# Kernel optimization log

Measured on AMD Instinct MI355X. Metric: run time of the kernel, lower is better.

The kernel has to match this reference:

```python
import jax, jax.numpy as jnp
import numpy as np

N = 100000   # nodes
E = 1600000  # edges
H = 150      # hidden_dim
G = 256      # num graphs in batch
L = 5        # num_layers
GATE_H = 200


def setup_inputs() -> dict:
    key = jax.random.key(0)
    ks = jax.random.split(key, 12)
    s = lambda k, shape, fan: jax.random.normal(k, shape, dtype=jnp.float32) / np.sqrt(fan)
    return {
        "x": jax.random.normal(ks[0], (N, H), dtype=jnp.float32),
        "edge_index": jax.random.randint(ks[1], (2, E), 0, N, dtype=jnp.int64),
        "batch": jnp.sort(jax.random.randint(ks[2], (N,), 0, G, dtype=jnp.int64)),
        "W": s(ks[3], (L, H, H), H),              # GatedGraphConv per-layer weight
        "w_ih": s(ks[4], (3 * H, H), H),           # GRUCell input weights (r,z,n)
        "w_hh": s(ks[5], (3 * H, H), H),
        "b_ih": jnp.zeros((3 * H,), jnp.float32),
        "b_hh": jnp.zeros((3 * H,), jnp.float32),
        "gw1": s(ks[6], (H, GATE_H), H),           # gate_nn Linear(150,200)
        "gb1": jnp.zeros((GATE_H,), jnp.float32),
        "gw2": s(ks[7], (GATE_H, 1), GATE_H),      # gate_nn Linear(200,1)
        "gb2": jnp.zeros((1,), jnp.float32),
    }


def _gru_cell(m, h, w_ih, w_hh, b_ih, b_hh):
    gi = m @ w_ih.T + b_ih   # [N, 3H]
    gh = h @ w_hh.T + b_hh
    ir, iz, inn = jnp.split(gi, 3, axis=-1)
    hr, hz, hn = jnp.split(gh, 3, axis=-1)
    r = jax.nn.sigmoid(ir + hr)
    z = jax.nn.sigmoid(iz + hz)
    n = jnp.tanh(inn + r * hn)
    return (1.0 - z) * n + z * h


def reference(x, edge_index, batch, W, w_ih, w_hh, b_ih, b_hh, gw1, gb1, gw2, gb2):
    src, dst = edge_index[0], edge_index[1]
    h = x
    # GatedGraphConv: per layer, linear transform, scatter_add aggregation, GRU update
    for i in range(L):
        m = h @ W[i]                                   # [N, H]
        agg = jax.ops.segment_sum(m[src], dst, num_segments=N)  # scatter_add over edges
        h = _gru_cell(agg, h, w_ih, w_hh, b_ih, b_hh)
    # GlobalAttention readout
    gate = jnp.tanh(h @ gw1 + gb1) @ gw2 + gb2          # [N, 1]
    gmax = jax.ops.segment_max(gate, batch, num_segments=G)    # [G, 1]
    gate = jnp.exp(gate - gmax[batch])
    gsum = jax.ops.segment_sum(gate, batch, num_segments=G)    # [G, 1]
    gate = gate / (gsum[batch] + 1e-16)                 # segment softmax
    out = jax.ops.segment_sum(gate * h, batch, num_segments=G)  # [G, H]
    return out, gate
```

## Files before the change

### kernel.cpp

```cpp
#include <hip/hip_runtime.h>
#include <math.h>

#define NN 100000
#define NE 1600000
#define H 150
#define NG 256
#define NL 5
#define GH 200
#define HS 160
#define LS 168
#define CHN 1563
#define CH2 782
#define SNB 98
#define CSRMAX 2304000

typedef unsigned short u16;
typedef unsigned int   u32;
typedef __attribute__((ext_vector_type(8))) short bf16x8;
typedef __attribute__((ext_vector_type(4))) float f32x4;

__device__ __forceinline__ float bf2f(u32 lo16){ u32 t = lo16 << 16; return __builtin_bit_cast(float, t); }
__device__ __forceinline__ u16 f2bf(float f){
  u32 u = __builtin_bit_cast(u32, f);
  u += 0x7fffu + ((u >> 16) & 1u);
  return (u16)(u >> 16);
}
__device__ __forceinline__ u32 pack2(float a, float b){ return (u32)f2bf(a) | ((u32)f2bf(b) << 16); }
__device__ __forceinline__ float fast_sig(float x){
  float e = __expf(-x);
  return __builtin_amdgcn_rcpf(1.f + e);
}
__device__ __forceinline__ float fast_tanh(float x){
  float cx = fminf(fmaxf(x, -15.f), 15.f);
  float e = __expf(2.f*cx);
  return (e - 1.f) * __builtin_amdgcn_rcpf(e + 1.f);
}

__global__ void k_hist(const int* __restrict__ ed, int* __restrict__ cnt){
  int e = blockIdx.x*256 + threadIdx.x;
  if (e < NE) atomicAdd(&cnt[ed[e]], 1);
}

__global__ __launch_bounds__(256) void k_scan1(const int* __restrict__ cnt, int* __restrict__ part){
  __shared__ int red[256];
  const int b = blockIdx.x, tid = threadIdx.x;
  const int base = b*1024;
  int s = 0;
  #pragma unroll
  for (int i = 0; i < 4; ++i){
    int idx = base + tid + i*256;
    int v = (idx < NN) ? cnt[idx] : 0;
    s += (v + 7) & ~7;
  }
  red[tid] = s; __syncthreads();
  for (int st = 128; st >= 1; st >>= 1){
    if (tid < st) red[tid] += red[tid+st];
    __syncthreads();
  }
  if (tid == 0) part[b] = red[0];
}

__global__ void k_scan2(int* __restrict__ part){
  const int t = threadIdx.x;
  int v0 = (2*t   < SNB) ? part[2*t]   : 0;
  int v1 = (2*t+1 < SNB) ? part[2*t+1] : 0;
  int s = v0 + v1, x = s;
  #pragma unroll
  for (int off = 1; off < 64; off <<= 1){
    int tt = __shfl_up(x, off);
    if (t >= off) x += tt;
  }
  int excl = x - s;
  if (2*t   < SNB) part[2*t]   = excl;
  if (2*t+1 < SNB) part[2*t+1] = excl + v0;
}

__global__ __launch_bounds__(1024) void k_scan3(const int* __restrict__ cnt,
        const int* __restrict__ part, int* __restrict__ rowptr, int* __restrict__ cursor){
  __shared__ int wsum[16];
  const int b = blockIdx.x, tid = threadIdx.x;
  const int wid = tid >> 6, lane = tid & 63;
  const int idx = b*1024 + tid;
  int c = (idx < NN) ? cnt[idx] : 0;
  int v = (c + 7) & ~7;
  int x = v;
  #pragma unroll
  for (int off = 1; off < 64; off <<= 1){
    int t = __shfl_up(x, off);
    if (lane >= off) x += t;
  }
  if (lane == 63) wsum[wid] = x;
  __syncthreads();
  if (tid < 16){
    int s = wsum[tid];
    int y = s;
    #pragma unroll
    for (int off = 1; off < 16; off <<= 1){
      int t = __shfl_up(y, off);
      if (tid >= off) y += t;
    }
    wsum[tid] = y - s;
  }
  __syncthreads();
  if (idx < NN){
    int incl = part[b] + wsum[wid] + x;
    rowptr[idx+1] = incl;
    cursor[idx]   = incl - v;
  }
  if (idx == 0) rowptr[0] = 0;
}

__global__ __launch_bounds__(256) void k_pre(int* __restrict__ csr){
  int i = (blockIdx.x*256 + threadIdx.x)*4;
  int4 v = {NN, NN, NN, NN};
  *(int4*)&csr[i] = v;
}

__global__ void k_fill(const int* __restrict__ es, const int* __restrict__ ed,
                       int* __restrict__ cursor, int* __restrict__ csr){
  int e = blockIdx.x*256 + threadIdx.x;
  if (e < NE){
    int pos = atomicAdd(&cursor[ed[e]], 1);
    csr[pos] = es[e];
  }
}

__global__ __launch_bounds__(256) void k_wc(const float* __restrict__ W,
        const float* __restrict__ wih, float* __restrict__ Wc){
  int idx = blockIdx.x*256 + threadIdx.x;
  if (idx >= NL*H*450) return;
  int l = idx / (H*450);
  int rem = idx - l*H*450;
  int k = rem / 450;
  int j = rem - k*450;
  const float* Wr = W   + (size_t)l*H*H + (size_t)k*H;
  const float* wr = wih + (size_t)j*H;
  float acc = 0.f;
  for (int t = 0; t < H; ++t) acc = fmaf(Wr[t], wr[t], acc);
  Wc[idx] = acc;
}

__global__ void k_packi(const float* __restrict__ Wc, short* __restrict__ wbi){
  int idx = blockIdx.x*256 + threadIdx.x;
  int li = idx & 511;
  int q = idx >> 9;
  int mat = q % 3; q /= 3;
  int ks = q % 5;  q /= 5;
  int ct = q % 10; int l = q / 10;
  int lane = li >> 3, j = li & 7;
  int k = ks*32 + ((lane >> 4) << 3) + j;
  int col = ct*16 + (lane & 15);
  float v = (k < H && col < H) ? Wc[(size_t)l*H*450 + (size_t)k*450 + mat*H + col] : 0.f;
  wbi[idx] = (short)f2bf(v);
}

__global__ void k_packh(const float* __restrict__ whh, short* __restrict__ wbh){
  int idx = blockIdx.x*256 + threadIdx.x;
  int li = idx & 511;
  int q = idx >> 9;
  int mat = q % 3; q /= 3;
  int ks = q % 5;  int ct = q / 5;
  int lane = li >> 3, j = li & 7;
  int k = ks*32 + ((lane >> 4) << 3) + j;
  int col = ct*16 + (lane & 15);
  float v = (k < H && col < H) ? whh[(size_t)(mat*H + col)*H + k] : 0.f;
  wbh[idx] = (short)f2bf(v);
}

__global__ void k_packg(const float* __restrict__ gw1, short* __restrict__ gw1b){
  int idx = blockIdx.x*256 + threadIdx.x;
  int li = idx & 511;
  int q = idx >> 9;
  int ks = q % 5;  int ct = q / 5;
  int lane = li >> 3, j = li & 7;
  int k = ks*32 + ((lane >> 4) << 3) + j;
  int col = ct*16 + (lane & 15);
  float v = (k < H && col < GH) ? gw1[(size_t)k*GH + col] : 0.f;
  gw1b[idx] = (short)f2bf(v);
}

__global__ void k_cvt(const float* __restrict__ x, short* __restrict__ hb){
  int idx = blockIdx.x*256 + threadIdx.x;
  if (idx >= NN*80) return;
  int n = idx / 80, c2 = idx - n*80;
  int c = c2*2;
  float lo = (c   < H) ? x[(size_t)n*H + c]   : 0.f;
  float hi = (c+1 < H) ? x[(size_t)n*H + c+1] : 0.f;
  ((u32*)hb)[idx] = (u32)f2bf(lo) | ((u32)f2bf(hi) << 16);
}

__global__ void k_zrow(short* __restrict__ a, short* __restrict__ b){
  int t = threadIdx.x;
  if (t < 80){
    ((u32*)a)[(size_t)NN*80 + t] = 0u;
    ((u32*)b)[(size_t)NN*80 + t] = 0u;
  }
}

__global__ __launch_bounds__(256) void k_gather(const short* __restrict__ hb,
        const int* __restrict__ rowptr, const int* __restrict__ csr,
        short* __restrict__ aggb){
  const int lane = threadIdx.x & 63;
  const int n = blockIdx.x*4 + (threadIdx.x >> 6);
  if (n >= NN) return;
  const int s0 = rowptr[n], s1 = rowptr[n+1];
  const u32* h32 = (const u32*)hb;
  const bool ext = lane < 16;
  float x0=0.f, x1=0.f, y0=0.f, y1=0.f;
  for (int j = s0; j < s1; j += 8){
    int4 ia = *(const int4*)&csr[j];
    int4 ib = *(const int4*)&csr[j+4];
    const u32* r0 = h32 + (size_t)ia.x*80;
    const u32* r1 = h32 + (size_t)ia.y*80;
    const u32* r2 = h32 + (size_t)ia.z*80;
    const u32* r3 = h32 + (size_t)ia.w*80;
    const u32* r4 = h32 + (size_t)ib.x*80;
    const u32* r5 = h32 + (size_t)ib.y*80;
    const u32* r6 = h32 + (size_t)ib.z*80;
    const u32* r7 = h32 + (size_t)ib.w*80;
    u32 v0 = r0[lane], v1 = r1[lane], v2 = r2[lane], v3 = r3[lane];
    u32 v4 = r4[lane], v5 = r5[lane], v6 = r6[lane], v7 = r7[lane];
    u32 u0=0,u1=0,u2=0,u3=0,u4=0,u5=0,u6=0,u7=0;
    if (ext){
      u0 = r0[64+lane]; u1 = r1[64+lane]; u2 = r2[64+lane]; u3 = r3[64+lane];
      u4 = r4[64+lane]; u5 = r5[64+lane]; u6 = r6[64+lane]; u7 = r7[64+lane];
    }
    x0 += bf2f(v0 & 0xffffu) + bf2f(v1 & 0xffffu) + bf2f(v2 & 0xffffu) + bf2f(v3 & 0xffffu)
        + bf2f(v4 & 0xffffu) + bf2f(v5 & 0xffffu) + bf2f(v6 & 0xffffu) + bf2f(v7 & 0xffffu);
    x1 += bf2f(v0 >> 16) + bf2f(v1 >> 16) + bf2f(v2 >> 16) + bf2f(v3 >> 16)
        + bf2f(v4 >> 16) + bf2f(v5 >> 16) + bf2f(v6 >> 16) + bf2f(v7 >> 16);
    if (ext){
      y0 += bf2f(u0 & 0xffffu) + bf2f(u1 & 0xffffu) + bf2f(u2 & 0xffffu) + bf2f(u3 & 0xffffu)
          + bf2f(u4 & 0xffffu) + bf2f(u5 & 0xffffu) + bf2f(u6 & 0xffffu) + bf2f(u7 & 0xffffu);
      y1 += bf2f(u0 >> 16) + bf2f(u1 >> 16) + bf2f(u2 >> 16) + bf2f(u3 >> 16)
          + bf2f(u4 >> 16) + bf2f(u5 >> 16) + bf2f(u6 >> 16) + bf2f(u7 >> 16);
    }
  }
  u32* o = (u32*)aggb + (size_t)n*80;
  o[lane] = pack2(x0, x1);
  if (ext) o[64+lane] = pack2(y0, y1);
}

__global__ __launch_bounds__(256, 2) void k_gru(
    const short* __restrict__ aggb, const short* __restrict__ hbc,
    short* __restrict__ hbn,
    const short* __restrict__ wbi_l, const short* __restrict__ wbh,
    const float* __restrict__ bih, const float* __restrict__ bhh){
  __shared__ short sB[30*512];
  const int tid = threadIdx.x;
  const int w = tid >> 6, lane = tid & 63;
  const int l16 = lane & 15, g = lane >> 4, g8 = g*8;
  const int row0 = blockIdx.x*128 + w*32;

  bf16x8 fA[2][5], fH[2][5];
  #pragma unroll
  for (int t = 0; t < 2; ++t){
    const int r = row0 + t*16 + l16;
    const bool rv = r < NN;
    #pragma unroll
    for (int ks = 0; ks < 5; ++ks){
      bf16x8 va = {0,0,0,0,0,0,0,0}, vh = {0,0,0,0,0,0,0,0};
      if (rv){
        va = *(const bf16x8*)&aggb[(size_t)r*HS + ks*32 + g8];
        vh = *(const bf16x8*)&hbc [(size_t)r*HS + ks*32 + g8];
      }
      fA[t][ks] = va; fH[t][ks] = vh;
    }
  }

  bf16x8 pr[8];
  #pragma unroll
  for (int k2 = 0; k2 < 8; ++k2){
    int u = tid + k2*256;
    if (u < 1920){
      int s = u >> 6, e = u & 63;
      const short* src = (s < 15) ? (wbi_l + s*512 + e*8)
                                  : (wbh  + (s-15)*512 + e*8);
      pr[k2] = *(const bf16x8*)src;
    }
  }

  for (int ct = 0; ct < 10; ++ct){
    __syncthreads();
    #pragma unroll
    for (int k2 = 0; k2 < 8; ++k2){
      int u = tid + k2*256;
      if (u < 1920) *(bf16x8*)&sB[u*8] = pr[k2];
    }
    __syncthreads();
    if (ct < 9){
      const int cto = (ct+1)*7680;
      #pragma unroll
      for (int k2 = 0; k2 < 8; ++k2){
        int u = tid + k2*256;
        if (u < 1920){
          int s = u >> 6, e = u & 63;
          const short* src = (s < 15) ? (wbi_l + cto + s*512 + e*8)
                                      : (wbh  + cto + (s-15)*512 + e*8);
          pr[k2] = *(const bf16x8*)src;
        }
      }
    }

    const int col = ct*16 + l16;
    const bool cv = col < H;
    const float bir = cv ? bih[col] : 0.f, biz = cv ? bih[H+col] : 0.f, bin_ = cv ? bih[2*H+col] : 0.f;
    const float bhr = cv ? bhh[col] : 0.f, bhz = cv ? bhh[H+col] : 0.f, bhn  = cv ? bhh[2*H+col] : 0.f;

    f32x4 ai[2][3], ah[2][3];
    #pragma unroll
    for (int t = 0; t < 2; ++t)
      #pragma unroll
      for (int m = 0; m < 3; ++m){ ai[t][m] = (f32x4){0,0,0,0}; ah[t][m] = (f32x4){0,0,0,0}; }

    #pragma unroll
    for (int ks = 0; ks < 5; ++ks){
      bf16x8 bi0 = *(const bf16x8*)&sB[(ks*3+0)*512 + lane*8];
      bf16x8 bi1 = *(const bf16x8*)&sB[(ks*3+1)*512 + lane*8];
      bf16x8 bi2 = *(const bf16x8*)&sB[(ks*3+2)*512 + lane*8];
      bf16x8 bh0 = *(const bf16x8*)&sB[(15+ks*3+0)*512 + lane*8];
      bf16x8 bh1 = *(const bf16x8*)&sB[(15+ks*3+1)*512 + lane*8];
      bf16x8 bh2 = *(const bf16x8*)&sB[(15+ks*3+2)*512 + lane*8];
      #pragma unroll
      for (int t = 0; t < 2; ++t){
        ai[t][0] = __builtin_amdgcn_mfma_f32_16x16x32_bf16(fA[t][ks], bi0, ai[t][0], 0,0,0);
        ai[t][1] = __builtin_amdgcn_mfma_f32_16x16x32_bf16(fA[t][ks], bi1, ai[t][1], 0,0,0);
        ai[t][2] = __builtin_amdgcn_mfma_f32_16x16x32_bf16(fA[t][ks], bi2, ai[t][2], 0,0,0);
        ah[t][0] = __builtin_amdgcn_mfma_f32_16x16x32_bf16(fH[t][ks], bh0, ah[t][0], 0,0,0);
        ah[t][1] = __builtin_amdgcn_mfma_f32_16x16x32_bf16(fH[t][ks], bh1, ah[t][1], 0,0,0);
        ah[t][2] = __builtin_amdgcn_mfma_f32_16x16x32_bf16(fH[t][ks], bh2, ah[t][2], 0,0,0);
      }
    }

    if (cv){
      #pragma unroll
      for (int t = 0; t < 2; ++t){
        #pragma unroll
        for (int r = 0; r < 4; ++r){
          int grow = row0 + t*16 + g*4 + r;
          if (grow < NN){
            float rr = fast_sig(ai[t][0][r]+bir + ah[t][0][r]+bhr);
            float zz = fast_sig(ai[t][1][r]+biz + ah[t][1][r]+bhz);
            float nn = fast_tanh(ai[t][2][r]+bin_ + rr*(ah[t][2][r]+bhn));
            float hold = bf2f((u32)(u16)hbc[(size_t)grow*HS + col]);
            float hnew = (1.f-zz)*nn + zz*hold;
            hbn[(size_t)grow*HS + col] = (short)f2bf(hnew);
          }
        }
      }
    }
  }
}

__global__ __launch_bounds__(256) void k_gatepre(const short* __restrict__ hb,
      const short* __restrict__ gw1b, const float* __restrict__ gb1,
      const float* __restrict__ gw2, const float* __restrict__ gb2,
      float* __restrict__ gbuf){
  __shared__ short sh[64*LS];
  __shared__ float part[4][4][4][4];
  const int tid = threadIdx.x;
  const int w = tid >> 6, lane = tid & 63;
  const int l16 = lane & 15, g = lane >> 4, g8 = g*8;
  const int chunk = blockIdx.x, row0 = chunk*64;

  for (int i = tid; i < 64*20; i += 256){
    int r = i/20, c = i - r*20;
    int gr = row0 + r;
    bf16x8 v = {0,0,0,0,0,0,0,0};
    if (gr < NN) v = *(const bf16x8*)&hb[(size_t)gr*HS + c*8];
    *(bf16x8*)&sh[r*LS + c*8] = v;
  }
  __syncthreads();

  float acc[4][4];
  #pragma unroll
  for (int rt=0; rt<4; ++rt){
    #pragma unroll
    for (int r=0; r<4; ++r) acc[rt][r] = 0.f;
  }
  for (int ct = w; ct < 13; ct += 4){
    bf16x8 B[5];
    const short* p = gw1b + (size_t)(ct*5)*512 + lane*8;
    #pragma unroll
    for (int ks = 0; ks < 5; ++ks) B[ks] = *(const bf16x8*)&p[ks*512];
    int col = ct*16 + l16;
    bool cv = col < GH;
    float g2 = cv ? gw2[col] : 0.f;
    float b1 = cv ? gb1[col] : 0.f;
    #pragma unroll
    for (int rt = 0; rt < 4; ++rt){
      f32x4 d = {0,0,0,0};
      #pragma unroll
      for (int ks = 0; ks < 5; ++ks){
        bf16x8 aH = *(const bf16x8*)&sh[(rt*16 + l16)*LS + ks*32 + g8];
        d = __builtin_amdgcn_mfma_f32_16x16x32_bf16(aH, B[ks], d, 0,0,0);
      }
      if (cv){
        #pragma unroll
        for (int r = 0; r < 4; ++r) acc[rt][r] += fast_tanh(d[r] + b1) * g2;
      }
    }
  }
  #pragma unroll
  for (int rt = 0; rt < 4; ++rt){
    #pragma unroll
    for (int r = 0; r < 4; ++r){
      float v = acc[rt][r];
      v += __shfl_xor(v, 1); v += __shfl_xor(v, 2);
      v += __shfl_xor(v, 4); v += __shfl_xor(v, 8);
      if (l16 == 0) part[w][rt][g][r] = v;
    }
  }
  __syncthreads();
  if (tid < 64){
    int rt = tid >> 4, gg = (tid >> 2) & 3, r = tid & 3;
    int grow = row0 + tid;
    if (grow < NN)
      gbuf[grow] = part[0][rt][gg][r] + part[1][rt][gg][r]
                 + part[2][rt][gg][r] + part[3][rt][gg][r] + gb2[0];
  }
}

__global__ __launch_bounds__(256) void k_readout(float* __restrict__ gatebuf,
    const short* __restrict__ hb, const int* __restrict__ batch,
    float* __restrict__ out, float* __restrict__ gate_out){
  const int g = blockIdx.x;
  const int tid = threadIdx.x;
  int lo=0, hi=NN;
  while (lo<hi){ int mid=(lo+hi)>>1; if (batch[mid] < g) lo=mid+1; else hi=mid; }
  const int start = lo;
  hi = NN;
  while (lo<hi){ int mid=(lo+hi)>>1; if (batch[mid] < g+1) lo=mid+1; else hi=mid; }
  const int end = lo;

  __shared__ float red[256];
  __shared__ float s_max, s_inv;
  float mx = -INFINITY;
  for (int n = start+tid; n < end; n += 256) mx = fmaxf(mx, gatebuf[n]);
  red[tid]=mx; __syncthreads();
  for (int s=128; s>=1; s>>=1){ if (tid<s) red[tid]=fmaxf(red[tid],red[tid+s]); __syncthreads(); }
  if (tid==0) s_max = red[0];
  __syncthreads();
  const float gmax = s_max;
  float sum = 0.f;
  for (int n = start+tid; n < end; n += 256){
    float e = expf(gatebuf[n]-gmax);
    gatebuf[n] = e;
    sum += e;
  }
  red[tid]=sum; __syncthreads();
  for (int s=128; s>=1; s>>=1){ if (tid<s) red[tid]+=red[tid+s]; __syncthreads(); }
  if (tid==0) s_inv = 1.0f/(red[0] + 1e-16f);
  __syncthreads();
  const float inv = s_inv;
  for (int n = start+tid; n < end; n += 256) gate_out[n] = gatebuf[n]*inv;
  if (tid < 80){
    const u32* h32 = (const u32*)hb;
    float acc0 = 0.f, acc1 = 0.f;
    for (int n = start; n < end; ++n){
      u32 v = h32[(size_t)n*80 + tid];
      float gv = gatebuf[n];
      acc0 = fmaf(gv, bf2f(v & 0xffffu), acc0);
      acc1 = fmaf(gv, bf2f(v >> 16),     acc1);
    }
    int c0 = 2*tid, c1 = 2*tid + 1;
    if (c0 < H) out[g*H + c0] = acc0*inv;
    if (c1 < H) out[g*H + c1] = acc1*inv;
  }
}

extern "C" void kernel_launch(void* const* d_in, const int* in_sizes, int n_in,
                              void* d_out, int out_size, void* d_ws, size_t ws_size,
                              hipStream_t stream) {
  (void)in_sizes; (void)n_in; (void)out_size; (void)ws_size;
  const float* x    = (const float*)d_in[0];
  const int*   eidx = (const int*)d_in[1];
  const int*   batch= (const int*)d_in[2];
  const float* W    = (const float*)d_in[3];
  const float* wih  = (const float*)d_in[4];
  const float* whh  = (const float*)d_in[5];
  const float* bih  = (const float*)d_in[6];
  const float* bhh  = (const float*)d_in[7];
  const float* gw1  = (const float*)d_in[8];
  const float* gb1  = (const float*)d_in[9];
  const float* gw2  = (const float*)d_in[10];
  const float* gb2  = (const float*)d_in[11];

  float* out      = (float*)d_out;
  float* gate_out = out + NG*H;

  char* p = (char*)d_ws;
  float* gbuf  = (float*)p;  p += (size_t)NN*4;
  float* Wc    = (float*)p;  p += (size_t)NL*H*450*4;
  short* hb0   = (short*)p;  p += (size_t)(NN+1)*HS*2;
  short* hb1   = (short*)p;  p += (size_t)(NN+1)*HS*2;
  short* aggb  = (short*)p;  p += (size_t)NN*HS*2;
  short* wbi   = (short*)p;  p += (size_t)NL*76800*2;
  short* wbh   = (short*)p;  p += (size_t)76800*2;
  short* gw1b  = (short*)p;  p += (size_t)33280*2;
  int*   cnt   = (int*)p;    p += (size_t)NN*4;
  int*   rowptr= (int*)p;    p += (size_t)(NN+1)*4;
  int*   cursor= (int*)p;    p += (size_t)NN*4;
  int*   csr   = (int*)p;    p += (size_t)CSRMAX*4;
  int*   spart = (int*)p;    p += (size_t)SNB*4;

  const int* esrc = eidx;
  const int* edst = eidx + NE;

  hipMemsetAsync(cnt, 0, sizeof(int)*NN, stream);
  k_hist<<<(NE+255)/256, 256, 0, stream>>>(edst, cnt);
  k_scan1<<<SNB, 256, 0, stream>>>(cnt, spart);
  k_scan2<<<1, 64, 0, stream>>>(spart);
  k_scan3<<<SNB, 1024, 0, stream>>>(cnt, spart, rowptr, cursor);
  k_pre <<<CSRMAX/1024, 256, 0, stream>>>(csr);
  k_fill<<<(NE+255)/256, 256, 0, stream>>>(esrc, edst, cursor, csr);

  k_wc   <<<(NL*H*450+255)/256, 256, 0, stream>>>(W, wih, Wc);
  k_packi<<<1500, 256, 0, stream>>>(Wc, wbi);
  k_packh<<<300,  256, 0, stream>>>(whh, wbh);
  k_packg<<<130,  256, 0, stream>>>(gw1, gw1b);

  k_cvt<<<(NN*80+255)/256, 256, 0, stream>>>(x, hb0);
  k_zrow<<<1, 128, 0, stream>>>(hb0, hb1);

  for (int l = 0; l < NL; ++l){
    short* cur  = (l & 1) ? hb1 : hb0;
    short* next = (l & 1) ? hb0 : hb1;
    k_gather<<<NN/4, 256, 0, stream>>>(cur, rowptr, csr, aggb);
    k_gru<<<CH2, 256, 0, stream>>>(aggb, cur, next,
                                   wbi + (size_t)l*76800, wbh, bih, bhh);
  }
  k_gatepre<<<CHN, 256, 0, stream>>>(hb1, gw1b, gb1, gw2, gb2, gbuf);
  k_readout<<<NG, 256, 0, stream>>>(gbuf, hb1, batch, out, gate_out);
}
```

Measured before the change: 1.241 ms.

## Bucket edges by destination before CSR fill; double-buffer GRU weight tiles

```diff
diff --git a/kernel.cpp b/kernel.cpp
--- a/kernel.cpp
+++ b/kernel.cpp
@@ -13,6 +13,8 @@
 #define CH2 782
 #define SNB 98
 #define CSRMAX 2304000
+#define NB 196
+#define EBLK 782
 
 typedef unsigned short u16;
 typedef unsigned int   u32;
@@ -116,12 +118,84 @@
   *(int4*)&csr[i] = v;
 }
 
-__global__ void k_fill(const int* __restrict__ es, const int* __restrict__ ed,
-                       int* __restrict__ cursor, int* __restrict__ csr){
+__global__ __launch_bounds__(256) void k_bhist(const int* __restrict__ ed, int* __restrict__ bcnt){
+  __shared__ int bh[NB];
+  const int tid = threadIdx.x;
+  for (int i = tid; i < NB; i += 256) bh[i] = 0;
+  __syncthreads();
+  const int base = blockIdx.x*2048;
+  #pragma unroll
+  for (int i = 0; i < 8; ++i){
+    int e = base + i*256 + tid;
+    if (e < NE) atomicAdd(&bh[ed[e] >> 9], 1);
+  }
+  __syncthreads();
+  for (int i = tid; i < NB; i += 256) if (bh[i]) atomicAdd(&bcnt[i], bh[i]);
+}
+
+__global__ void k_bscan(const int* __restrict__ bcnt, int* __restrict__ bcur){
+  __shared__ int ws[4];
+  const int t = threadIdx.x, lane = t & 63, w = t >> 6;
+  int v = (t < NB) ? bcnt[t] : 0;
+  int x = v;
+  #pragma unroll
+  for (int off = 1; off < 64; off <<= 1){
+    int tt = __shfl_up(x, off);
+    if (lane >= off) x += tt;
+  }
+  if (lane == 63) ws[w] = x;
+  __syncthreads();
+  if (t == 0){
+    int s = 0;
+    #pragma unroll
+    for (int i = 0; i < 4; ++i){ int tmp = ws[i]; ws[i] = s; s += tmp; }
+  }
+  __syncthreads();
+  if (t < NB) bcur[t] = ws[w] + x - v;
+}
+
+__global__ __launch_bounds__(256) void k_bscatter(const int* __restrict__ es,
+        const int* __restrict__ ed, int* __restrict__ bcur, int2* __restrict__ ebuf){
+  __shared__ int lh[NB];
+  __shared__ int lbase[NB];
+  const int tid = threadIdx.x;
+  for (int i = tid; i < NB; i += 256) lh[i] = 0;
+  __syncthreads();
+  const int base = blockIdx.x*2048;
+  u32 meta[8]; int srcs[8], dsts[8];
+  #pragma unroll
+  for (int i = 0; i < 8; ++i){
+    int e = base + i*256 + tid;
+    if (e < NE){
+      int d = ed[e];
+      int b = d >> 9;
+      int lr = atomicAdd(&lh[b], 1);
+      meta[i] = ((u32)b << 16) | (u32)lr;
+      srcs[i] = es[e]; dsts[i] = d;
+    } else meta[i] = 0xffffffffu;
+  }
+  __syncthreads();
+  for (int i = tid; i < NB; i += 256){
+    int c = lh[i];
+    lbase[i] = c ? atomicAdd(&bcur[i], c) : 0;
+  }
+  __syncthreads();
+  #pragma unroll
+  for (int i = 0; i < 8; ++i){
+    if (meta[i] != 0xffffffffu){
+      int b = meta[i] >> 16, lr = meta[i] & 0xffff;
+      ebuf[lbase[b] + lr] = make_int2(srcs[i], dsts[i]);
+    }
+  }
+}
+
+__global__ void k_fill2(const int2* __restrict__ ebuf, int* __restrict__ cursor,
+                        int* __restrict__ csr){
   int e = blockIdx.x*256 + threadIdx.x;
   if (e < NE){
-    int pos = atomicAdd(&cursor[ed[e]], 1);
-    csr[pos] = es[e];
+    int2 sd = ebuf[e];
+    int pos = atomicAdd(&cursor[sd.y], 1);
+    csr[pos] = sd.x;
   }
 }
 
@@ -246,7 +320,7 @@
     short* __restrict__ hbn,
     const short* __restrict__ wbi_l, const short* __restrict__ wbh,
     const float* __restrict__ bih, const float* __restrict__ bhh){
-  __shared__ short sB[30*512];
+  __shared__ short sB[2][15360];
   const int tid = threadIdx.x;
   const int w = tid >> 6, lane = tid & 63;
   const int l16 = lane & 15, g = lane >> 4, g8 = g*8;
@@ -279,14 +353,14 @@
       pr[k2] = *(const bf16x8*)src;
     }
   }
+  #pragma unroll
+  for (int k2 = 0; k2 < 8; ++k2){
+    int u = tid + k2*256;
+    if (u < 1920) *(bf16x8*)&sB[0][u*8] = pr[k2];
+  }
 
   for (int ct = 0; ct < 10; ++ct){
-    __syncthreads();
-    #pragma unroll
-    for (int k2 = 0; k2 < 8; ++k2){
-      int u = tid + k2*256;
-      if (u < 1920) *(bf16x8*)&sB[u*8] = pr[k2];
-    }
+    const int cur = ct & 1;
     __syncthreads();
     if (ct < 9){
       const int cto = (ct+1)*7680;
@@ -313,14 +387,15 @@
       #pragma unroll
       for (int m = 0; m < 3; ++m){ ai[t][m] = (f32x4){0,0,0,0}; ah[t][m] = (f32x4){0,0,0,0}; }
 
+    const short* sbc = sB[cur];
     #pragma unroll
     for (int ks = 0; ks < 5; ++ks){
-      bf16x8 bi0 = *(const bf16x8*)&sB[(ks*3+0)*512 + lane*8];
-      bf16x8 bi1 = *(const bf16x8*)&sB[(ks*3+1)*512 + lane*8];
-      bf16x8 bi2 = *(const bf16x8*)&sB[(ks*3+2)*512 + lane*8];
-      bf16x8 bh0 = *(const bf16x8*)&sB[(15+ks*3+0)*512 + lane*8];
-      bf16x8 bh1 = *(const bf16x8*)&sB[(15+ks*3+1)*512 + lane*8];
-      bf16x8 bh2 = *(const bf16x8*)&sB[(15+ks*3+2)*512 + lane*8];
+      bf16x8 bi0 = *(const bf16x8*)&sbc[(ks*3+0)*512 + lane*8];
+      bf16x8 bi1 = *(const bf16x8*)&sbc[(ks*3+1)*512 + lane*8];
+      bf16x8 bi2 = *(const bf16x8*)&sbc[(ks*3+2)*512 + lane*8];
+      bf16x8 bh0 = *(const bf16x8*)&sbc[(15+ks*3+0)*512 + lane*8];
+      bf16x8 bh1 = *(const bf16x8*)&sbc[(15+ks*3+1)*512 + lane*8];
+      bf16x8 bh2 = *(const bf16x8*)&sbc[(15+ks*3+2)*512 + lane*8];
       #pragma unroll
       for (int t = 0; t < 2; ++t){
         ai[t][0] = __builtin_amdgcn_mfma_f32_16x16x32_bf16(fA[t][ks], bi0, ai[t][0], 0,0,0);
@@ -329,6 +404,14 @@
         ah[t][0] = __builtin_amdgcn_mfma_f32_16x16x32_bf16(fH[t][ks], bh0, ah[t][0], 0,0,0);
         ah[t][1] = __builtin_amdgcn_mfma_f32_16x16x32_bf16(fH[t][ks], bh1, ah[t][1], 0,0,0);
         ah[t][2] = __builtin_amdgcn_mfma_f32_16x16x32_bf16(fH[t][ks], bh2, ah[t][2], 0,0,0);
+      }
+    }
+
+    if (ct < 9){
+      #pragma unroll
+      for (int k2 = 0; k2 < 8; ++k2){
+        int u = tid + k2*256;
+        if (u < 1920) *(bf16x8*)&sB[cur^1][u*8] = pr[k2];
       }
     }
 
@@ -503,17 +586,24 @@
   int*   cursor= (int*)p;    p += (size_t)NN*4;
   int*   csr   = (int*)p;    p += (size_t)CSRMAX*4;
   int*   spart = (int*)p;    p += (size_t)SNB*4;
+  int*   bcnt  = (int*)p;    p += (size_t)NB*4;
+  int*   bcur  = (int*)p;    p += (size_t)NB*4;
+  int2*  ebuf  = (int2*)p;   p += (size_t)NE*8;
 
   const int* esrc = eidx;
   const int* edst = eidx + NE;
 
   hipMemsetAsync(cnt, 0, sizeof(int)*NN, stream);
+  hipMemsetAsync(bcnt, 0, sizeof(int)*NB, stream);
   k_hist<<<(NE+255)/256, 256, 0, stream>>>(edst, cnt);
   k_scan1<<<SNB, 256, 0, stream>>>(cnt, spart);
   k_scan2<<<1, 64, 0, stream>>>(spart);
   k_scan3<<<SNB, 1024, 0, stream>>>(cnt, spart, rowptr, cursor);
   k_pre <<<CSRMAX/1024, 256, 0, stream>>>(csr);
-  k_fill<<<(NE+255)/256, 256, 0, stream>>>(esrc, edst, cursor, csr);
+  k_bhist<<<EBLK, 256, 0, stream>>>(edst, bcnt);
+  k_bscan<<<1, 256, 0, stream>>>(bcnt, bcur);
+  k_bscatter<<<EBLK, 256, 0, stream>>>(esrc, edst, bcur, ebuf);
+  k_fill2<<<(NE+255)/256, 256, 0, stream>>>(ebuf, cursor, csr);
 
   k_wc   <<<(NL*H*450+255)/256, 256, 0, stream>>>(W, wih, Wc);
   k_packi<<<1500, 256, 0, stream>>>(Wc, wbi);
```

Result: no change. 1.232 ms (-0.7%).
